# Optimization experiments

Hardware: AMD Instinct MI355X
Metric: run time of the kernel (lower is better)

The kernel has to match this reference:

```python
import jax, jax.numpy as jnp
import numpy as np

B, T, E, H = 2, 4096, 1024, 16
D = E // H  # head dim = 64

def setup_inputs() -> dict:
    key = jax.random.key(0)
    ks = jax.random.split(key, 5)
    x = jax.random.normal(ks[0], (B, T, E), dtype=jnp.float32)
    # torch Linear(n_embed, 3*n_embed): y = x @ W.T + b ; we store W already transposed as (E, 3E)
    w_qkv = jax.random.normal(ks[1], (E, 3 * E), dtype=jnp.float32) * (1.0 / np.sqrt(E))
    b_qkv = jax.random.normal(ks[2], (3 * E,), dtype=jnp.float32) * 0.02
    w_out = jax.random.normal(ks[3], (E, E), dtype=jnp.float32) * (1.0 / np.sqrt(E))
    b_out = jax.random.normal(ks[4], (E,), dtype=jnp.float32) * 0.02
    return {"x": x, "w_qkv": w_qkv, "b_qkv": b_qkv, "w_out": w_out, "b_out": b_out}

def reference(x, w_qkv, b_qkv, w_out, b_out):
    b, t, e = x.shape
    qkv = x @ w_qkv + b_qkv                      # (B,T,3E)
    # matches torch: view(B,T,H,3D) then chunk(3, dim=-1)
    qkv = qkv.reshape(b, t, H, 3 * D)
    q, k, v = jnp.split(qkv, 3, axis=-1)          # each (B,T,H,D)
    q = q.transpose(0, 2, 1, 3)                   # (B,H,T,D)
    k = k.transpose(0, 2, 1, 3)
    v = v.transpose(0, 2, 1, 3)
    scores = jnp.einsum('bhqd,bhkd->bhqk', q, k) / jnp.sqrt(jnp.float32(D))
    causal = jnp.tril(jnp.ones((t, t), dtype=bool))
    scores = jnp.where(causal, scores, jnp.float32(-jnp.inf))
    w = jax.nn.softmax(scores, axis=-1)           # (B,H,T,T)
    out = jnp.einsum('bhqk,bhkd->bhqd', w, v)     # (B,H,T,D)
    out = out.transpose(0, 2, 1, 3).reshape(b, t, e)
    return out @ w_out + b_out
```

## Files before the change

### kernel.cpp

```cpp
#include <hip/hip_runtime.h>
#include <stdint.h>
#include <math.h>

#define T_SEQ 4096

typedef __attribute__((ext_vector_type(8))) short short8;
typedef __attribute__((ext_vector_type(4))) float f32x4;
typedef __attribute__((ext_vector_type(16))) float f32x16;
typedef __attribute__((ext_vector_type(4))) uint16_t u16x4;

__device__ __forceinline__ uint16_t f2bf(float f) {
  uint32_t u = __float_as_uint(f);
  u += 0x7FFFu + ((u >> 16) & 1u);
  return (uint16_t)(u >> 16);
}

__device__ __forceinline__ void gload_lds16(const uint16_t* g, uint16_t* l) {
  __builtin_amdgcn_global_load_lds(
      (const __attribute__((address_space(1))) void*)g,
      (__attribute__((address_space(3))) void*)l, 16, 0, 0);
}

__global__ void __launch_bounds__(256) k_cvt(const float* __restrict__ in,
                                             uint16_t* __restrict__ out, int n4) {
  int i = blockIdx.x * 256 + threadIdx.x;
  if (i >= n4) return;
  float4 v = reinterpret_cast<const float4*>(in)[i];
  u16x4 o = { f2bf(v.x), f2bf(v.y), f2bf(v.z), f2bf(v.w) };
  reinterpret_cast<u16x4*>(out)[i] = o;
}

__global__ void __launch_bounds__(256) k_tc(const float* __restrict__ w,
                                            uint16_t* __restrict__ wt, int R, int C) {
  __shared__ uint16_t tile[32][33];
  int tx = threadIdx.x & 31, ty = threadIdx.x >> 5;
  int r0 = blockIdx.y * 32, c0 = blockIdx.x * 32;
#pragma unroll
  for (int i = 0; i < 4; i++)
    tile[ty + 8 * i][tx] = f2bf(w[(size_t)(r0 + ty + 8 * i) * C + c0 + tx]);
  __syncthreads();
#pragma unroll
  for (int i = 0; i < 4; i++)
    wt[(size_t)(c0 + ty + 8 * i) * R + r0 + tx] = tile[tx][ty + 8 * i];
}

__global__ void __launch_bounds__(256) k_vt(const uint16_t* __restrict__ qkv,
                                            uint16_t* __restrict__ vT) {
  __shared__ uint16_t tile[64][65];
  const int bh = blockIdx.y, b = bh >> 4, h = bh & 15;
  const int t0 = blockIdx.x * 64;
  const int tid = threadIdx.x;
  const int r = tid >> 3, c8 = tid & 7;
  const uint16_t* src = qkv + ((size_t)b * T_SEQ + t0) * 3072 + h * 192 + 128;
#pragma unroll
  for (int i = 0; i < 2; i++) {
    int row = r + 32 * i;
    short8 v = *reinterpret_cast<const short8*>(src + (size_t)row * 3072 + c8 * 8);
#pragma unroll
    for (int j = 0; j < 8; j++) tile[row][c8 * 8 + j] = (uint16_t)v[j];
  }
  __syncthreads();
  uint16_t* dst = vT + ((size_t)bh * 64) * T_SEQ + t0;
#pragma unroll
  for (int i = 0; i < 2; i++) {
    int d = r + 32 * i;
    short8 v;
#pragma unroll
    for (int j = 0; j < 8; j++) v[j] = (short)tile[c8 * 8 + j][d];
    *reinterpret_cast<short8*>(dst + (size_t)d * T_SEQ + c8 * 8) = v;
  }
}

template <int BF16_OUT>
__global__ void __launch_bounds__(256, 2) k_gemm(const uint16_t* __restrict__ A,
                                                 const uint16_t* __restrict__ BT,
                                                 const float* __restrict__ bias,
                                                 void* __restrict__ Cout,
                                                 int M, int N, int K) {
  __shared__ __align__(16) uint16_t As[2][128 * 64];
  __shared__ __align__(16) uint16_t Bs[2][128 * 64];
  const int tid = threadIdx.x;
  const int lane = tid & 63, wid = tid >> 6;
  const int lr = lane & 15, lg = lane >> 4;
  const int wr = wid >> 1, wc = wid & 1;

  const int bid = blockIdx.x;
  const int cpx = gridDim.x >> 3;
  const int lin = (bid & 7) * cpx + (bid >> 3);
  const int mt = M >> 7;
  const int n0 = (lin / mt) * 128;
  const int m0 = (lin % mt) * 128;

  const f32x4 vzero = {0.f, 0.f, 0.f, 0.f};
  f32x4 acc[4][4];
#pragma unroll
  for (int i = 0; i < 4; i++)
#pragma unroll
    for (int j = 0; j < 4; j++) acc[i][j] = vzero;

  const int sl = lane >> 3, ss = lane & 7;
  const int swzs = (ss ^ sl) * 8;
  const uint16_t* a0 = A + (size_t)(m0 + wid * 32 + sl) * K + swzs;
  const uint16_t* b0 = BT + (size_t)(n0 + wid * 32 + sl) * K + swzs;
  const size_t r8 = (size_t)8 * K;

#define STAGE(bsel, t)                                                   \
  do {                                                                   \
    const int koff_ = (t) * 64;                                          \
    gload_lds16(a0 + koff_,          &As[bsel][(wid * 32 + 0) * 64]);    \
    gload_lds16(a0 + r8 + koff_,     &As[bsel][(wid * 32 + 8) * 64]);    \
    gload_lds16(a0 + 2 * r8 + koff_, &As[bsel][(wid * 32 + 16) * 64]);   \
    gload_lds16(a0 + 3 * r8 + koff_, &As[bsel][(wid * 32 + 24) * 64]);   \
    gload_lds16(b0 + koff_,          &Bs[bsel][(wid * 32 + 0) * 64]);    \
    gload_lds16(b0 + r8 + koff_,     &Bs[bsel][(wid * 32 + 8) * 64]);    \
    gload_lds16(b0 + 2 * r8 + koff_, &Bs[bsel][(wid * 32 + 16) * 64]);   \
    gload_lds16(b0 + 3 * r8 + koff_, &Bs[bsel][(wid * 32 + 24) * 64]);   \
  } while (0)

  const int nt = K >> 6;
  const int fsw = lr & 7;
  STAGE(0, 0);
  STAGE(1, 1);
  __syncthreads();

  for (int t = 0; t < nt; ++t) {
    const int cur = t & 1;
#pragma unroll
    for (int ks = 0; ks < 2; ++ks) {
      const int col = (((ks * 4 + lg) ^ fsw) * 8);
      short8 af[4], bf[4];
#pragma unroll
      for (int mi = 0; mi < 4; ++mi)
        af[mi] = *reinterpret_cast<const short8*>(
            &As[cur][(wr * 64 + mi * 16 + lr) * 64 + col]);
#pragma unroll
      for (int nj = 0; nj < 4; ++nj)
        bf[nj] = *reinterpret_cast<const short8*>(
            &Bs[cur][(wc * 64 + nj * 16 + lr) * 64 + col]);
      __builtin_amdgcn_s_setprio(1);
#pragma unroll
      for (int mi = 0; mi < 4; ++mi)
#pragma unroll
        for (int nj = 0; nj < 4; ++nj)
          acc[mi][nj] = __builtin_amdgcn_mfma_f32_16x16x32_bf16(af[mi], bf[nj], acc[mi][nj], 0, 0, 0);
      __builtin_amdgcn_s_setprio(0);
    }
    __syncthreads();
    if (t + 2 < nt) STAGE(cur, t + 2);
  }
#undef STAGE

#pragma unroll
  for (int nj = 0; nj < 4; nj++) {
    int col = n0 + wc * 64 + nj * 16 + lr;
    float bv = bias[col];
#pragma unroll
    for (int mi = 0; mi < 4; mi++) {
      int rowb = m0 + wr * 64 + mi * 16 + lg * 4;
#pragma unroll
      for (int r = 0; r < 4; r++) {
        float v = acc[mi][nj][r] + bv;
        if (BF16_OUT)
          ((uint16_t*)Cout)[(size_t)(rowb + r) * N + col] = f2bf(v);
        else
          ((float*)Cout)[(size_t)(rowb + r) * N + col] = v;
      }
    }
  }
}

__global__ void __launch_bounds__(512, 1) k_gemm256p(const uint16_t* __restrict__ A,
                                                     const uint16_t* __restrict__ BT,
                                                     const float* __restrict__ bias,
                                                     uint16_t* __restrict__ Cout,
                                                     int M, int N, int K) {
  __shared__ __align__(16) uint16_t As[2][256 * 64];
  __shared__ __align__(16) uint16_t Bs[2][256 * 64];
  const int tid = threadIdx.x;
  const int lane = tid & 63, wid = tid >> 6;
  const int lr = lane & 15, lg = lane >> 4;
  const int wr = wid >> 2, wc = wid & 3;

  const int bid = blockIdx.x;
  const int cpx = gridDim.x >> 3;
  const int lin = (bid & 7) * cpx + (bid >> 3);
  const int mt = M >> 8;
  const int n0 = (lin / mt) * 256;
  const int m0 = (lin % mt) * 256;

  const f32x4 vzero = {0.f, 0.f, 0.f, 0.f};
  f32x4 acc[8][4];
#pragma unroll
  for (int i = 0; i < 8; i++)
#pragma unroll
    for (int j = 0; j < 4; j++) acc[i][j] = vzero;

  const int sl = lane >> 3, ss = lane & 7;
  const int swzs = (ss ^ sl) * 8;
  const uint16_t* a0 = A + (size_t)(m0 + wid * 32 + sl) * K + swzs;
  const uint16_t* b0 = BT + (size_t)(n0 + wid * 32 + sl) * K + swzs;
  const size_t r8 = (size_t)8 * K;

#define STAGE_A(bsel, t)                                                  \
  do {                                                                    \
    const int ko_ = (t) * 64;                                             \
    gload_lds16(a0 + ko_,          &As[bsel][(wid * 32 + 0) * 64]);       \
    gload_lds16(a0 + r8 + ko_,     &As[bsel][(wid * 32 + 8) * 64]);       \
    gload_lds16(a0 + 2 * r8 + ko_, &As[bsel][(wid * 32 + 16) * 64]);      \
    gload_lds16(a0 + 3 * r8 + ko_, &As[bsel][(wid * 32 + 24) * 64]);      \
  } while (0)
#define STAGE_B(bsel, t)                                                  \
  do {                                                                    \
    const int ko_ = (t) * 64;                                             \
    gload_lds16(b0 + ko_,          &Bs[bsel][(wid * 32 + 0) * 64]);       \
    gload_lds16(b0 + r8 + ko_,     &Bs[bsel][(wid * 32 + 8) * 64]);       \
    gload_lds16(b0 + 2 * r8 + ko_, &Bs[bsel][(wid * 32 + 16) * 64]);      \
    gload_lds16(b0 + 3 * r8 + ko_, &Bs[bsel][(wid * 32 + 24) * 64]);      \
  } while (0)

  const int nt = K >> 6;
  const int fsw = lr & 7;
  STAGE_A(0, 0);
  STAGE_B(0, 0);
  __syncthreads();

  for (int t = 0; t < nt; ++t) {
    const int cur = t & 1;
    const int nxt = cur ^ 1;

    short8 bf[4][2];
#pragma unroll
    for (int nj = 0; nj < 4; ++nj)
#pragma unroll
      for (int ks = 0; ks < 2; ++ks)
        bf[nj][ks] = *reinterpret_cast<const short8*>(
            &Bs[cur][(wc * 64 + nj * 16 + lr) * 64 + (((ks * 4 + lg) ^ fsw) * 8)]);

#define PHASE(mi0)                                                            \
  do {                                                                        \
    short8 af0k0 = *reinterpret_cast<const short8*>(                          \
        &As[cur][(wr * 128 + (mi0) * 16 + lr) * 64 + (((0 * 4 + lg) ^ fsw) * 8)]); \
    short8 af0k1 = *reinterpret_cast<const short8*>(                          \
        &As[cur][(wr * 128 + (mi0) * 16 + lr) * 64 + (((1 * 4 + lg) ^ fsw) * 8)]); \
    short8 af1k0 = *reinterpret_cast<const short8*>(                          \
        &As[cur][(wr * 128 + (mi0 + 1) * 16 + lr) * 64 + (((0 * 4 + lg) ^ fsw) * 8)]); \
    short8 af1k1 = *reinterpret_cast<const short8*>(                          \
        &As[cur][(wr * 128 + (mi0 + 1) * 16 + lr) * 64 + (((1 * 4 + lg) ^ fsw) * 8)]); \
    __builtin_amdgcn_s_setprio(1);                                            \
    _Pragma("unroll")                                                         \
    for (int nj = 0; nj < 4; ++nj) {                                          \
      acc[mi0][nj] = __builtin_amdgcn_mfma_f32_16x16x32_bf16(af0k0, bf[nj][0], acc[mi0][nj], 0, 0, 0); \
      acc[mi0][nj] = __builtin_amdgcn_mfma_f32_16x16x32_bf16(af0k1, bf[nj][1], acc[mi0][nj], 0, 0, 0); \
      acc[mi0 + 1][nj] = __builtin_amdgcn_mfma_f32_16x16x32_bf16(af1k0, bf[nj][0], acc[mi0 + 1][nj], 0, 0, 0); \
      acc[mi0 + 1][nj] = __builtin_amdgcn_mfma_f32_16x16x32_bf16(af1k1, bf[nj][1], acc[mi0 + 1][nj], 0, 0, 0); \
    }                                                                         \
    __builtin_amdgcn_s_setprio(0);                                            \
  } while (0)

    if (t + 1 < nt) STAGE_A(nxt, t + 1);
    PHASE(0);
    if (t + 1 < nt) STAGE_B(nxt, t + 1);
    PHASE(2);
    PHASE(4);
    PHASE(6);
#undef PHASE

    __syncthreads();
  }
#undef STAGE_A
#undef STAGE_B

#pragma unroll
  for (int nj = 0; nj < 4; nj++) {
    int col = n0 + wc * 64 + nj * 16 + lr;
    float bv = bias[col];
#pragma unroll
    for (int mi = 0; mi < 8; mi++) {
      int rowb = m0 + wr * 128 + mi * 16 + lg * 4;
#pragma unroll
      for (int r = 0; r < 4; r++)
        Cout[(size_t)(rowb + r) * N + col] = f2bf(acc[mi][nj][r] + bv);
    }
  }
}

#define KVB 64
__global__ void __launch_bounds__(256) k_attn(const uint16_t* __restrict__ qkv,
                                              const uint16_t* __restrict__ vT,
                                              uint16_t* __restrict__ out) {
  __shared__ __align__(16) char lds[32768];
  const int tid = threadIdx.x;
  const int lane = tid & 63, wid = tid >> 6;
  const int l31 = lane & 31, hi = lane >> 5;
  const int hi4 = hi * 4;

  const int bid = blockIdx.x;
  const int xcd = bid & 7, j = bid >> 3;
  const int bh = xcd * 4 + (j & 3);
  const int qt = 31 - (j >> 2);
  const int b = bh >> 4, h = bh & 15;
  const int q0 = qt * 128;
  const size_t rowbase = (size_t)b * T_SEQ;
  const int hoff = h * 192;
  const uint16_t* Kg = qkv + rowbase * 3072 + hoff + 64;
  const uint16_t* Vg = vT + (size_t)bh * 64 * T_SEQ;

  const int sr = tid >> 3, sc = tid & 7;
  const int wsw = (sc ^ (sr & 7)) * 16;
  const float C_SC = 0.180336881f;

  int rslot[4];
#pragma unroll
  for (int c = 0; c < 4; c++) rslot[c] = (((2 * c + hi) ^ (lane & 7)) << 4);
  const int rowb128 = l31 * 128;

  const int qrow = q0 + wid * 32 + l31;
  short8 qf[4];
#pragma unroll
  for (int ks = 0; ks < 4; ks++) {
    short8 raw = *reinterpret_cast<const short8*>(
        qkv + (rowbase + qrow) * 3072 + hoff + hi * 8 + ks * 16);
    union { short8 s; uint32_t u[4]; } pk;
#pragma unroll
    for (int e = 0; e < 4; e++) {
      float f0 = __uint_as_float(((uint32_t)(uint16_t)raw[2 * e]) << 16) * C_SC;
      float f1 = __uint_as_float(((uint32_t)(uint16_t)raw[2 * e + 1]) << 16) * C_SC;
      asm("v_cvt_pk_bf16_f32 %0, %1, %2" : "=v"(pk.u[e]) : "v"(f0), "v"(f1));
    }
    qf[ks] = pk.s;
  }

  f32x16 o0, o1, zero16;
#pragma unroll
  for (int i = 0; i < 16; i++) zero16[i] = 0.f;
  o0 = zero16; o1 = zero16;
  float lpart = 0.f;

  const int nkt = 2 * qt + 2;
  const int qwmax = q0 + wid * 32 + 31;

  short8 rk0, rk1, rv0, rv1;
  rk0 = *reinterpret_cast<const short8*>(Kg + (size_t)sr * 3072 + sc * 8);
  rk1 = *reinterpret_cast<const short8*>(Kg + (size_t)(sr + 32) * 3072 + sc * 8);
  rv0 = *reinterpret_cast<const short8*>(Vg + (size_t)sr * T_SEQ + sc * 8);
  rv1 = *reinterpret_cast<const short8*>(Vg + (size_t)(sr + 32) * T_SEQ + sc * 8);
  {
    char* kb0 = lds;
    char* vb0 = lds + 16384;
    *reinterpret_cast<short8*>(kb0 + sr * 128 + wsw) = rk0;
    *reinterpret_cast<short8*>(kb0 + (sr + 32) * 128 + wsw) = rk1;
    *reinterpret_cast<short8*>(vb0 + sr * 128 + wsw) = rv0;
    *reinterpret_cast<short8*>(vb0 + (sr + 32) * 128 + wsw) = rv1;
  }
  if (nkt > 1) {
    rk0 = *reinterpret_cast<const short8*>(Kg + (size_t)(KVB + sr) * 3072 + sc * 8);
    rk1 = *reinterpret_cast<const short8*>(Kg + (size_t)(KVB + sr + 32) * 3072 + sc * 8);
    rv0 = *reinterpret_cast<const short8*>(Vg + (size_t)sr * T_SEQ + KVB + sc * 8);
    rv1 = *reinterpret_cast<const short8*>(Vg + (size_t)(sr + 32) * T_SEQ + KVB + sc * 8);
  }

  for (int kt = 0; kt < nkt; kt++) {
    __syncthreads();
    if (kt + 1 < nkt) {
      const int nsel = (kt + 1) & 1;
      char* kb = lds + (nsel ? 8192 : 0);
      char* vb = lds + 16384 + (nsel ? 8192 : 0);
      *reinterpret_cast<short8*>(kb + sr * 128 + wsw) = rk0;
      *reinterpret_cast<short8*>(kb + (sr + 32) * 128 + wsw) = rk1;
      *reinterpret_cast<short8*>(vb + sr * 128 + wsw) = rv0;
      *reinterpret_cast<short8*>(vb + (sr + 32) * 128 + wsw) = rv1;
      if (kt + 2 < nkt) {
        int k0n = (kt + 2) * KVB;
        rk0 = *reinterpret_cast<const short8*>(Kg + (size_t)(k0n + sr) * 3072 + sc * 8);
        rk1 = *reinterpret_cast<const short8*>(Kg + (size_t)(k0n + sr + 32) * 3072 + sc * 8);
        rv0 = *reinterpret_cast<const short8*>(Vg + (size_t)sr * T_SEQ + k0n + sc * 8);
        rv1 = *reinterpret_cast<const short8*>(Vg + (size_t)(sr + 32) * T_SEQ + k0n + sc * 8);
      }
    }

    if (kt * KVB <= qwmax) {
      const int csel = kt & 1;
      char* kcur = lds + (csel ? 8192 : 0);
      char* vcur = lds + 16384 + (csel ? 8192 : 0);
      const int ktb = kt * KVB;
      const bool notfull = (ktb + 63 > q0 + wid * 32);

      f32x16 s0 = zero16, s1 = zero16;
      __builtin_amdgcn_s_setprio(1);
#pragma unroll
      for (int ks = 0; ks < 4; ks++) {
        short8 kf0 = *reinterpret_cast<const short8*>(kcur + rowb128 + rslot[ks]);
        short8 kf1 = *reinterpret_cast<const short8*>(kcur + 4096 + rowb128 + rslot[ks]);
        s0 = __builtin_amdgcn_mfma_f32_32x32x16_bf16(kf0, qf[ks], s0, 0, 0, 0);
        s1 = __builtin_amdgcn_mfma_f32_32x32x16_bf16(kf1, qf[ks], s1, 0, 0, 0);
      }
      __builtin_amdgcn_s_setprio(0);

      uint32_t u0[8], u1[8];
#define SMAX_KB(SV, KB, U)                                                    \
  do {                                                                        \
    _Pragma("unroll")                                                         \
    for (int r = 0; r < 16; r++) {                                            \
      float v = SV[r];                                                        \
      if (notfull) {                                                          \
        int key = ktb + (KB) * 32 + (r & 3) + 8 * (r >> 2) + hi4;             \
        if (key > qrow) v = -INFINITY;                                        \
      }                                                                       \
      float p = __builtin_amdgcn_exp2f(v);                                    \
      SV[r] = p;                                                              \
      lpart += p;                                                             \
    }                                                                         \
    _Pragma("unroll")                                                         \
    for (int jj = 0; jj < 8; jj++)                                            \
      asm("v_cvt_pk_bf16_f32 %0, %1, %2"                                      \
          : "=v"(U[jj]) : "v"(SV[2 * jj]), "v"(SV[2 * jj + 1]));              \
    asm volatile("v_permlane32_swap_b32 %0, %1" : "+v"(U[0]), "+v"(U[2]));    \
    asm volatile("v_permlane32_swap_b32 %0, %1" : "+v"(U[1]), "+v"(U[3]));    \
    asm volatile("v_permlane32_swap_b32 %0, %1" : "+v"(U[4]), "+v"(U[6]));    \
    asm volatile("v_permlane32_swap_b32 %0, %1" : "+v"(U[5]), "+v"(U[7]));    \
  } while (0)

      SMAX_KB(s0, 0, u0);
      SMAX_KB(s1, 1, u1);
#undef SMAX_KB

      union { uint32_t u[4]; short8 s; } pf;
      __builtin_amdgcn_s_setprio(1);
#pragma unroll
      for (int kv = 0; kv < 4; kv++) {
        if (kv == 0) { pf.u[0] = u0[0]; pf.u[1] = u0[1]; pf.u[2] = u0[2]; pf.u[3] = u0[3]; }
        else if (kv == 1) { pf.u[0] = u0[4]; pf.u[1] = u0[5]; pf.u[2] = u0[6]; pf.u[3] = u0[7]; }
        else if (kv == 2) { pf.u[0] = u1[0]; pf.u[1] = u1[1]; pf.u[2] = u1[2]; pf.u[3] = u1[3]; }
        else { pf.u[0] = u1[4]; pf.u[1] = u1[5]; pf.u[2] = u1[6]; pf.u[3] = u1[7]; }
        short8 vf0 = *reinterpret_cast<const short8*>(vcur + rowb128 + rslot[kv]);
        short8 vf1 = *reinterpret_cast<const short8*>(vcur + 4096 + rowb128 + rslot[kv]);
        o0 = __builtin_amdgcn_mfma_f32_32x32x16_bf16(vf0, pf.s, o0, 0, 0, 0);
        o1 = __builtin_amdgcn_mfma_f32_32x32x16_bf16(vf1, pf.s, o1, 0, 0, 0);
      }
      __builtin_amdgcn_s_setprio(0);
    }
  }

  __syncthreads();
  float ltot = lpart + __shfl_xor(lpart, 32);
  float inv = 1.0f / ltot;
  char* scrb = lds + wid * 8192;
#pragma unroll
  for (int g = 0; g < 4; g++) {
    f32x4 w0, w1;
#pragma unroll
    for (int e = 0; e < 4; e++) { w0[e] = o0[4 * g + e] * inv; w1[e] = o1[4 * g + e] * inv; }
    int s0i = 2 * g + hi, s1i = s0i + 8;
    *reinterpret_cast<f32x4*>(scrb + l31 * 256 + ((s0i ^ (l31 & 7)) << 4)) = w0;
    *reinterpret_cast<f32x4*>(scrb + l31 * 256 + ((s1i ^ (l31 & 7)) << 4)) = w1;
  }
  asm volatile("s_waitcnt lgkmcnt(0)" ::: "memory");
  __builtin_amdgcn_sched_barrier(0);
  {
    int row = lane >> 1, half = lane & 1;
    uint16_t tmp[32];
#pragma unroll
    for (int k = 0; k < 8; k++) {
      f32x4 vv = *reinterpret_cast<const f32x4*>(
          scrb + row * 256 + (((half * 8 + k) ^ (row & 7)) << 4));
#pragma unroll
      for (int e = 0; e < 4; e++) tmp[k * 4 + e] = f2bf(vv[e]);
    }
    uint16_t* op = out + (rowbase + q0 + wid * 32 + row) * 1024 + h * 64 + half * 32;
#pragma unroll
    for (int k = 0; k < 4; k++)
      *reinterpret_cast<short8*>(op + k * 8) = *reinterpret_cast<const short8*>(tmp + k * 8);
  }
}

extern "C" void kernel_launch(void* const* d_in, const int* in_sizes, int n_in,
                              void* d_out, int out_size, void* d_ws, size_t ws_size,
                              hipStream_t stream) {
  const float* x = (const float*)d_in[0];
  const float* w_qkv = (const float*)d_in[1];
  const float* b_qkv = (const float*)d_in[2];
  const float* w_out = (const float*)d_in[3];
  const float* b_out = (const float*)d_in[4];
  float* out = (float*)d_out;

  uint8_t* ws = (uint8_t*)d_ws;
  uint16_t* x_bf  = (uint16_t*)(ws);
  uint16_t* wqkvT = (uint16_t*)(ws + (16u << 20));
  uint16_t* woutT = (uint16_t*)(ws + (22u << 20));
  uint16_t* qkv   = (uint16_t*)(ws + (24u << 20));
  uint16_t* vTbuf = (uint16_t*)(ws + (72u << 20));
  uint16_t* attn_o = x_bf;

  k_cvt<<<8192, 256, 0, stream>>>(x, x_bf, 2097152);
  k_tc<<<dim3(96, 32), 256, 0, stream>>>(w_qkv, wqkvT, 1024, 3072);
  k_tc<<<dim3(32, 32), 256, 0, stream>>>(w_out, woutT, 1024, 1024);
  k_gemm256p<<<384, 512, 0, stream>>>(x_bf, wqkvT, b_qkv, qkv, 8192, 3072, 1024);
  k_vt<<<dim3(64, 32), 256, 0, stream>>>(qkv, vTbuf);
  k_attn<<<1024, 256, 0, stream>>>(qkv, vTbuf, attn_o);
  k_gemm<0><<<512, 256, 0, stream>>>(attn_o, woutT, b_out, out, 8192, 1024, 1024);
}
```

Baseline: 220.3 us.

## Replace output projection GEMM with 256x128-tile, 512-thread interleaved-prefetch kernel

The output projection GEMM moves from a 128x128 tile, 256-thread kernel with two-deep prefetch to a 256x128 tile, 512-thread kernel. The new kernel issues the next K-slice loads between MFMA phases, mirroring the QKV GEMM structure, to raise data reuse per block and overlap loads with compute. The grid drops to 256 blocks on 256 CUs with one block each, so there is no second resident block to hide latency, and the old kernel is deleted.

New measurement: 224.0 us. Within noise of the previous version (+1.7%).

```diff
diff --git a/kernel.cpp b/kernel.cpp
--- a/kernel.cpp
+++ b/kernel.cpp
@@ -68,104 +68,6 @@
 #pragma unroll
     for (int j = 0; j < 8; j++) v[j] = (short)tile[c8 * 8 + j][d];
     *reinterpret_cast<short8*>(dst + (size_t)d * T_SEQ + c8 * 8) = v;
-  }
-}
-
-template <int BF16_OUT>
-__global__ void __launch_bounds__(256, 2) k_gemm(const uint16_t* __restrict__ A,
-                                                 const uint16_t* __restrict__ BT,
-                                                 const float* __restrict__ bias,
-                                                 void* __restrict__ Cout,
-                                                 int M, int N, int K) {
-  __shared__ __align__(16) uint16_t As[2][128 * 64];
-  __shared__ __align__(16) uint16_t Bs[2][128 * 64];
-  const int tid = threadIdx.x;
-  const int lane = tid & 63, wid = tid >> 6;
-  const int lr = lane & 15, lg = lane >> 4;
-  const int wr = wid >> 1, wc = wid & 1;
-
-  const int bid = blockIdx.x;
-  const int cpx = gridDim.x >> 3;
-  const int lin = (bid & 7) * cpx + (bid >> 3);
-  const int mt = M >> 7;
-  const int n0 = (lin / mt) * 128;
-  const int m0 = (lin % mt) * 128;
-
-  const f32x4 vzero = {0.f, 0.f, 0.f, 0.f};
-  f32x4 acc[4][4];
-#pragma unroll
-  for (int i = 0; i < 4; i++)
-#pragma unroll
-    for (int j = 0; j < 4; j++) acc[i][j] = vzero;
-
-  const int sl = lane >> 3, ss = lane & 7;
-  const int swzs = (ss ^ sl) * 8;
-  const uint16_t* a0 = A + (size_t)(m0 + wid * 32 + sl) * K + swzs;
-  const uint16_t* b0 = BT + (size_t)(n0 + wid * 32 + sl) * K + swzs;
-  const size_t r8 = (size_t)8 * K;
-
-#define STAGE(bsel, t)                                                   \
-  do {                                                                   \
-    const int koff_ = (t) * 64;                                          \
-    gload_lds16(a0 + koff_,          &As[bsel][(wid * 32 + 0) * 64]);    \
-    gload_lds16(a0 + r8 + koff_,     &As[bsel][(wid * 32 + 8) * 64]);    \
-    gload_lds16(a0 + 2 * r8 + koff_, &As[bsel][(wid * 32 + 16) * 64]);   \
-    gload_lds16(a0 + 3 * r8 + koff_, &As[bsel][(wid * 32 + 24) * 64]);   \
-    gload_lds16(b0 + koff_,          &Bs[bsel][(wid * 32 + 0) * 64]);    \
-    gload_lds16(b0 + r8 + koff_,     &Bs[bsel][(wid * 32 + 8) * 64]);    \
-    gload_lds16(b0 + 2 * r8 + koff_, &Bs[bsel][(wid * 32 + 16) * 64]);   \
-    gload_lds16(b0 + 3 * r8 + koff_, &Bs[bsel][(wid * 32 + 24) * 64]);   \
-  } while (0)
-
-  const int nt = K >> 6;
-  const int fsw = lr & 7;
-  STAGE(0, 0);
-  STAGE(1, 1);
-  __syncthreads();
-
-  for (int t = 0; t < nt; ++t) {
-    const int cur = t & 1;
-#pragma unroll
-    for (int ks = 0; ks < 2; ++ks) {
-      const int col = (((ks * 4 + lg) ^ fsw) * 8);
-      short8 af[4], bf[4];
-#pragma unroll
-      for (int mi = 0; mi < 4; ++mi)
-        af[mi] = *reinterpret_cast<const short8*>(
-            &As[cur][(wr * 64 + mi * 16 + lr) * 64 + col]);
-#pragma unroll
-      for (int nj = 0; nj < 4; ++nj)
-        bf[nj] = *reinterpret_cast<const short8*>(
-            &Bs[cur][(wc * 64 + nj * 16 + lr) * 64 + col]);
-      __builtin_amdgcn_s_setprio(1);
-#pragma unroll
-      for (int mi = 0; mi < 4; ++mi)
-#pragma unroll
-        for (int nj = 0; nj < 4; ++nj)
-          acc[mi][nj] = __builtin_amdgcn_mfma_f32_16x16x32_bf16(af[mi], bf[nj], acc[mi][nj], 0, 0, 0);
-      __builtin_amdgcn_s_setprio(0);
-    }
-    __syncthreads();
-    if (t + 2 < nt) STAGE(cur, t + 2);
-  }
-#undef STAGE
-
-#pragma unroll
-  for (int nj = 0; nj < 4; nj++) {
-    int col = n0 + wc * 64 + nj * 16 + lr;
-    float bv = bias[col];
-#pragma unroll
-    for (int mi = 0; mi < 4; mi++) {
-      int rowb = m0 + wr * 64 + mi * 16 + lg * 4;
-#pragma unroll
-      for (int r = 0; r < 4; r++) {
-        float v = acc[mi][nj][r] + bv;
-        if (BF16_OUT)
-          ((uint16_t*)Cout)[(size_t)(rowb + r) * N + col] = f2bf(v);
-        else
-          ((float*)Cout)[(size_t)(rowb + r) * N + col] = v;
-      }
-    }
   }
 }
 
@@ -280,6 +182,119 @@
 #pragma unroll
       for (int r = 0; r < 4; r++)
         Cout[(size_t)(rowb + r) * N + col] = f2bf(acc[mi][nj][r] + bv);
+    }
+  }
+}
+
+__global__ void __launch_bounds__(512, 1) k_gemm2(const uint16_t* __restrict__ A,
+                                                  const uint16_t* __restrict__ BT,
+                                                  const float* __restrict__ bias,
+                                                  float* __restrict__ Cout,
+                                                  int M, int N, int K) {
+  __shared__ __align__(16) uint16_t As[2][256 * 64];
+  __shared__ __align__(16) uint16_t Bs[2][128 * 64];
+  const int tid = threadIdx.x;
+  const int lane = tid & 63, wid = tid >> 6;
+  const int lr = lane & 15, lg = lane >> 4;
+  const int wr = wid >> 2, wc = wid & 3;
+
+  const int bid = blockIdx.x;
+  const int cpx = gridDim.x >> 3;
+  const int lin = (bid & 7) * cpx + (bid >> 3);
+  const int mt = M >> 8;
+  const int n0 = (lin / mt) * 128;
+  const int m0 = (lin % mt) * 256;
+
+  const f32x4 vzero = {0.f, 0.f, 0.f, 0.f};
+  f32x4 acc[8][2];
+#pragma unroll
+  for (int i = 0; i < 8; i++)
+#pragma unroll
+    for (int j = 0; j < 2; j++) acc[i][j] = vzero;
+
+  const int sl = lane >> 3, ss = lane & 7;
+  const int swzs = (ss ^ sl) * 8;
+  const uint16_t* a0 = A + (size_t)(m0 + wid * 32 + sl) * K + swzs;
+  const uint16_t* b0 = BT + (size_t)(n0 + wid * 16 + sl) * K + swzs;
+  const size_t r8 = (size_t)8 * K;
+
+#define STAGE_A2(bsel, t)                                                 \
+  do {                                                                    \
+    const int ko_ = (t) * 64;                                             \
+    gload_lds16(a0 + ko_,          &As[bsel][(wid * 32 + 0) * 64]);       \
+    gload_lds16(a0 + r8 + ko_,     &As[bsel][(wid * 32 + 8) * 64]);       \
+    gload_lds16(a0 + 2 * r8 + ko_, &As[bsel][(wid * 32 + 16) * 64]);      \
+    gload_lds16(a0 + 3 * r8 + ko_, &As[bsel][(wid * 32 + 24) * 64]);      \
+  } while (0)
+#define STAGE_B2(bsel, t)                                                 \
+  do {                                                                    \
+    const int ko_ = (t) * 64;                                             \
+    gload_lds16(b0 + ko_,      &Bs[bsel][(wid * 16 + 0) * 64]);           \
+    gload_lds16(b0 + r8 + ko_, &Bs[bsel][(wid * 16 + 8) * 64]);           \
+  } while (0)
+
+  const int nt = K >> 6;
+  const int fsw = lr & 7;
+  STAGE_A2(0, 0);
+  STAGE_B2(0, 0);
+  __syncthreads();
+
+  for (int t = 0; t < nt; ++t) {
+    const int cur = t & 1;
+    const int nxt = cur ^ 1;
+
+    short8 bf[2][2];
+#pragma unroll
+    for (int nj = 0; nj < 2; ++nj)
+#pragma unroll
+      for (int ks = 0; ks < 2; ++ks)
+        bf[nj][ks] = *reinterpret_cast<const short8*>(
+            &Bs[cur][(wc * 32 + nj * 16 + lr) * 64 + (((ks * 4 + lg) ^ fsw) * 8)]);
+
+#define PHASE2(mi0)                                                           \
+  do {                                                                        \
+    short8 af0k0 = *reinterpret_cast<const short8*>(                          \
+        &As[cur][(wr * 128 + (mi0) * 16 + lr) * 64 + (((0 * 4 + lg) ^ fsw) * 8)]); \
+    short8 af0k1 = *reinterpret_cast<const short8*>(                          \
+        &As[cur][(wr * 128 + (mi0) * 16 + lr) * 64 + (((1 * 4 + lg) ^ fsw) * 8)]); \
+    short8 af1k0 = *reinterpret_cast<const short8*>(                          \
+        &As[cur][(wr * 128 + (mi0 + 1) * 16 + lr) * 64 + (((0 * 4 + lg) ^ fsw) * 8)]); \
+    short8 af1k1 = *reinterpret_cast<const short8*>(                          \
+        &As[cur][(wr * 128 + (mi0 + 1) * 16 + lr) * 64 + (((1 * 4 + lg) ^ fsw) * 8)]); \
+    __builtin_amdgcn_s_setprio(1);                                            \
+    _Pragma("unroll")                                                         \
+    for (int nj = 0; nj < 2; ++nj) {                                          \
+      acc[mi0][nj] = __builtin_amdgcn_mfma_f32_16x16x32_bf16(af0k0, bf[nj][0], acc[mi0][nj], 0, 0, 0); \
+      acc[mi0][nj] = __builtin_amdgcn_mfma_f32_16x16x32_bf16(af0k1, bf[nj][1], acc[mi0][nj], 0, 0, 0); \
+      acc[mi0 + 1][nj] = __builtin_amdgcn_mfma_f32_16x16x32_bf16(af1k0, bf[nj][0], acc[mi0 + 1][nj], 0, 0, 0); \
+      acc[mi0 + 1][nj] = __builtin_amdgcn_mfma_f32_16x16x32_bf16(af1k1, bf[nj][1], acc[mi0 + 1][nj], 0, 0, 0); \
+    }                                                                         \
+    __builtin_amdgcn_s_setprio(0);                                            \
+  } while (0)
+
+    if (t + 1 < nt) STAGE_A2(nxt, t + 1);
+    PHASE2(0);
+    if (t + 1 < nt) STAGE_B2(nxt, t + 1);
+    PHASE2(2);
+    PHASE2(4);
+    PHASE2(6);
+#undef PHASE2
+
+    __syncthreads();
+  }
+#undef STAGE_A2
+#undef STAGE_B2
+
+#pragma unroll
+  for (int nj = 0; nj < 2; nj++) {
+    int col = n0 + wc * 32 + nj * 16 + lr;
+    float bv = bias[col];
+#pragma unroll
+    for (int mi = 0; mi < 8; mi++) {
+      int rowb = m0 + wr * 128 + mi * 16 + lg * 4;
+#pragma unroll
+      for (int r = 0; r < 4; r++)
+        Cout[(size_t)(rowb + r) * N + col] = acc[mi][nj][r] + bv;
     }
   }
 }
@@ -497,5 +512,5 @@
   k_gemm256p<<<384, 512, 0, stream>>>(x_bf, wqkvT, b_qkv, qkv, 8192, 3072, 1024);
   k_vt<<<dim3(64, 32), 256, 0, stream>>>(qkv, vTbuf);
   k_attn<<<1024, 256, 0, stream>>>(qkv, vTbuf, attn_o);
-  k_gemm<0><<<512, 256, 0, stream>>>(attn_o, woutT, b_out, out, 8192, 1024, 1024);
-}
+  k_gemm2<<<256, 512, 0, stream>>>(attn_o, woutT, b_out, out, 8192, 1024, 1024);
+}
```
